# Kernel optimization log

Hardware: AMD Instinct MI355X
Metric: run time of the kernel (lower is better)

## Reference

```python
import jax, jax.numpy as jnp
import numpy as np
from jax import lax
jax.config.update('jax_enable_x64', True)

SR = 44100
BLOCK = 512
N_MELS = 80
N_ALLPASS = 256
N_HARM = 512
N_NOISE = 256
HID = 256
B = 16
NF = 400
T = NF * BLOCK
N_OUT = N_ALLPASS + N_HARM + N_NOISE


def upsample(sig, factor):
    # torch: interpolate(cat(sig, sig[-1:]), size=n*factor+1, mode='linear', align_corners=True)[:-1]
    b, n, c = sig.shape
    ext = jnp.concatenate([sig, sig[:, -1:]], axis=1)  # (b, n+1, c)
    w = (jnp.arange(factor, dtype=jnp.float32) / factor)[None, None, :, None]
    up = ext[:, :-1, None, :] * (1.0 - w) + ext[:, 1:, None, :] * w
    return up.reshape(b, n * factor, c)


def hann_periodic(n):
    return 0.5 - 0.5 * jnp.cos(2.0 * np.pi * jnp.arange(n, dtype=jnp.float32) / n)


def freq_impulse_response(mag, hann_window, half_width=None):
    # mag: (b, nf, m) complex -> ir: (b, nf, 2*(m-1)) in causal (rolled) form
    ir = jnp.fft.irfft(mag).astype(jnp.float32)
    n = ir.shape[-1]
    if hann_window:
        if half_width is None:
            w = jnp.roll(hann_periodic(n), n // 2)
            ir = jnp.roll(ir * w, n // 2, axis=-1)
        else:
            # dynamic hann window with per-frame half width (b, nf, 1)
            w = jnp.arange(-(n // 2), (n + 1) // 2, dtype=jnp.float32) / half_width
            w = jnp.where(w > 1.0, 0.0, w)
            w = (1.0 + jnp.cos(np.pi * w)) * 0.5
            ir = jnp.roll(ir, n // 2, axis=-1) * w
    else:
        ir = jnp.roll(ir, n // 2, axis=-1)
    return ir


def fft_convolve(audio, ir):
    b, t = audio.shape
    nf, ir_size = ir.shape[1], ir.shape[2]
    hop = t // nf
    frame = 2 * hop
    fft_size = frame + ir_size - 1
    chunks = jnp.pad(audio, ((0, 0), (hop, hop))).reshape(b, nf + 2, hop)
    frames = jnp.concatenate([chunks[:, :-1], chunks[:, 1:]], axis=-1)  # (b, nf+1, frame)
    bart = 1.0 - jnp.abs(2.0 * jnp.arange(frame, dtype=jnp.float32) / frame - 1.0)
    frames = frames * bart
    ir_ext = jnp.concatenate([ir, ir[:, -1:]], axis=1)  # repeat last IR frame
    out_f = jnp.fft.irfft(jnp.fft.rfft(frames, fft_size) * jnp.fft.rfft(ir_ext, fft_size), fft_size).astype(jnp.float32)
    n_out = nf + 1
    length = (n_out - 1) * hop + fft_size
    idx = (jnp.arange(n_out)[:, None] * hop + jnp.arange(fft_size)[None, :]).reshape(-1)
    out = jnp.zeros((b, length), jnp.float32).at[:, idx].add(out_f.reshape(b, -1))
    return out[:, hop:t + hop]


def conv1d_same(x, w, bias):
    y = lax.conv_general_dilated(x, w, (1,), [(1, 1)], dimension_numbers=('NCH', 'OIH', 'NCH'))
    return y + bias[None, :, None]


def mel2ctrl(mel, phase, conv1_w, conv1_b, gn_g, gn_b, conv2_w, conv2_b, phase_w, phase_b, ln_g, ln_b, out_w, out_b):
    h = conv1d_same(mel.transpose(0, 2, 1), conv1_w, conv1_b)  # (b, 256, nf)
    b, c, l = h.shape
    g = h.reshape(b, 4, c // 4, l)  # GroupNorm(4, 256)
    mu = g.mean((2, 3), keepdims=True)
    var = g.var((2, 3), keepdims=True)
    h = ((g - mu) / jnp.sqrt(var + 1e-5)).reshape(b, c, l)
    h = h * gn_g[None, :, None] + gn_b[None, :, None]
    h = jnp.where(h >= 0, h, 0.01 * h)  # LeakyReLU
    h = conv1d_same(h, conv2_w, conv2_b).transpose(0, 2, 1)  # (b, nf, 256)
    pe = jnp.concatenate([jnp.sin(phase), jnp.cos(phase)], axis=-1) @ phase_w.T + phase_b
    h = h + pe
    mu = h.mean(-1, keepdims=True)
    var = h.var(-1, keepdims=True)
    h = (h - mu) / jnp.sqrt(var + 1e-5) * ln_g + ln_b
    out = h @ out_w.T + out_b
    gd = out[..., :N_ALLPASS]
    hm = out[..., N_ALLPASS:N_ALLPASS + N_HARM]
    nm = out[..., N_ALLPASS + N_HARM:]
    return gd, hm, nm


def setup_inputs():
    key = jax.random.key(0)
    ks = jax.random.split(key, 8)
    s = 0.02
    return {
        'mel_frames': jax.random.normal(ks[0], (B, NF, N_MELS), jnp.float32),
        'f0_frames': jax.random.uniform(ks[1], (B, NF, 1), jnp.float32) * 400.0 + 100.0,
        'initial_phase': jnp.zeros((B, 1, 1), jnp.float32),
        'uniform_noise': jax.random.uniform(ks[2], (B, T), jnp.float32),
        'conv1_w': jax.random.normal(ks[3], (HID, N_MELS, 3), jnp.float32) * s,
        'conv1_b': jnp.zeros((HID,), jnp.float32),
        'gn_g': jnp.ones((HID,), jnp.float32),
        'gn_b': jnp.zeros((HID,), jnp.float32),
        'conv2_w': jax.random.normal(ks[4], (HID, HID, 3), jnp.float32) * s,
        'conv2_b': jnp.zeros((HID,), jnp.float32),
        'phase_w': jax.random.normal(ks[5], (HID, 2), jnp.float32) * s,
        'phase_b': jnp.zeros((HID,), jnp.float32),
        'ln_g': jnp.ones((HID,), jnp.float32),
        'ln_b': jnp.zeros((HID,), jnp.float32),
        'out_w': jax.random.normal(ks[6], (N_OUT, HID), jnp.float32) * s,
        'out_b': jnp.zeros((N_OUT,), jnp.float32),
    }


def reference(mel_frames, f0_frames, initial_phase, uniform_noise, conv1_w, conv1_b, gn_g, gn_b, conv2_w, conv2_b, phase_w, phase_b, ln_g, ln_b, out_w, out_b):
    f0 = upsample(f0_frames, BLOCK)  # (B, T, 1)
    # double-precision wrapped phase accumulation
    x = jnp.cumsum(f0.astype(jnp.float64) / SR, axis=1) + initial_phase.astype(jnp.float64) / (2.0 * np.pi)
    x = (x - jnp.round(x)).astype(jnp.float32)
    phase_frames = 2.0 * np.pi * x[:, ::BLOCK, :]  # (B, NF, 1)
    gd_raw, hm_raw, nm_raw = mel2ctrl(mel_frames, phase_frames, conv1_w, conv1_b, gn_g, gn_b, conv2_w, conv2_b, phase_w, phase_b, ln_g, ln_b, out_w, out_b)
    group_delay = np.pi * jnp.tanh(gd_raw)
    src_param = jnp.exp(hm_raw)
    noise_param = jnp.exp(nm_raw) / 128.0
    combtooth = jnp.sinc(SR * x / (f0 + 0.001))[..., 0]  # (B, T)
    allpass = jnp.exp(1j * jnp.cumsum(group_delay, axis=-1).astype(jnp.complex64))
    harmonic = fft_convolve(combtooth, freq_impulse_response(allpass, hann_window=False))
    half_width = 1.5 * SR / (f0_frames + 0.001)  # (B, NF, 1)
    harmonic = fft_convolve(harmonic, freq_impulse_response(src_param.astype(jnp.complex64), True, half_width))
    noise = uniform_noise * 2.0 - 1.0
    noise = fft_convolve(noise, freq_impulse_response(noise_param.astype(jnp.complex64), True, None))
    signal = harmonic + noise
    return signal, phase_frames, harmonic, noise
```

## Files before the change

### kernel.cpp

```cpp
#include <hip/hip_runtime.h>
#include <math.h>

#define BATCH 16
#define NF_ 400
#define TLEN 204800
#define NMELS 80
#define HID 256
#define SRD 44100.0

static constexpr size_t S_ = 1638400;
static constexpr size_t OFF_COMB = 0;
static constexpr size_t OFF_H1   = 2 * S_;
static constexpr size_t OFF_H2   = 3 * S_;
static constexpr size_t OFF_IR1  = 2 * S_;
static constexpr size_t OFF_PHI  = 4 * S_;
static constexpr size_t OFF_NSP  = 5 * S_;
static constexpr size_t OFF_HTMP = 4 * S_;
static constexpr size_t OFF_SRC  = 6 * S_;
static constexpr size_t OFF_IR3  = 6 * S_;
static constexpr size_t OFF_IR2  = 8 * S_;
static constexpr size_t OFF_FSUM = 12 * S_;
static constexpr size_t OFF_PREF = 12 * S_ + 12800;
static constexpr size_t OFF_GN   = 12 * S_ + 25600;

__device__ __forceinline__ float cs6_f0_at(const float* f0f, int b, int n, int k) {
    float a = f0f[b * NF_ + n];
    float c = f0f[b * NF_ + min(n + 1, NF_ - 1)];
    float w = (float)k * (1.0f / 512.0f);
    return __fadd_rn(__fmul_rn(a, 1.0f - w), __fmul_rn(c, w));
}

__global__ void cs6_fsum(const float* __restrict__ f0f, double* __restrict__ fsum) {
    int gid = blockIdx.x * blockDim.x + threadIdx.x;
    if (gid >= BATCH * NF_) return;
    int b = gid / NF_, n = gid % NF_;
    double s = 0.0;
    for (int k = 0; k < 512; ++k) s += (double)cs6_f0_at(f0f, b, n, k) / SRD;
    fsum[gid] = s;
}

__global__ void cs6_prefix(const double* __restrict__ fsum, double* __restrict__ pref) {
    int b = threadIdx.x;
    if (b >= BATCH) return;
    double run = 0.0;
    for (int n = 0; n < NF_; ++n) { pref[b * NF_ + n] = run; run += fsum[b * NF_ + n]; }
}

__global__ __launch_bounds__(512) void cs6_phase(const float* __restrict__ f0f,
        const float* __restrict__ ip, const double* __restrict__ pref,
        float* __restrict__ comb, float* __restrict__ phase_out) {
    __shared__ double sc[512];
    int b = blockIdx.x / NF_, n = blockIdx.x % NF_;
    int k = threadIdx.x;
    float f0 = cs6_f0_at(f0f, b, n, k);
    sc[k] = (double)f0 / SRD;
    __syncthreads();
    for (int off = 1; off < 512; off <<= 1) {
        double v = (k >= off) ? sc[k - off] : 0.0;
        __syncthreads();
        sc[k] += v;
        __syncthreads();
    }
    double xd = pref[b * NF_ + n] + sc[k] + (double)ip[b] / (2.0 * M_PI);
    xd -= rint(xd);
    float xf = (float)xd;
    double zd = 44100.0 * (double)xf / ((double)f0 + 0.001);
    double pz = M_PI * zd;
    comb[(size_t)b * TLEN + n * 512 + k] = (zd == 0.0) ? 1.0f : (float)(sin(pz) / pz);
    if (k == 0) phase_out[b * NF_ + n] = (float)(2.0 * M_PI * (double)xf);
}

__global__ __launch_bounds__(256) void cs6_conv1x3(const float* __restrict__ mel,
        const float* __restrict__ w1, const float* __restrict__ b1, float* __restrict__ h1) {
    __shared__ float m3[3][NMELS];
    int b = blockIdx.x / NF_, l = blockIdx.x % NF_;
    int tid = threadIdx.x;
    for (int i = tid; i < 3 * NMELS; i += 256) {
        int tap = i / NMELS, ic = i % NMELS;
        int li = l + tap - 1;
        m3[tap][ic] = (li >= 0 && li < NF_) ? mel[((size_t)b * NF_ + li) * NMELS + ic] : 0.0f;
    }
    __syncthreads();
    int oc = tid;
    double acc = (double)b1[oc];
    const float* wp = w1 + (size_t)oc * NMELS * 3;
    for (int ic = 0; ic < NMELS; ++ic)
        acc += (double)m3[0][ic] * (double)wp[ic * 3]
             + (double)m3[1][ic] * (double)wp[ic * 3 + 1]
             + (double)m3[2][ic] * (double)wp[ic * 3 + 2];
    h1[((size_t)b * NF_ + l) * HID + oc] = (float)acc;
}

__global__ __launch_bounds__(256) void cs6_gnstats(const float* __restrict__ h1, float* __restrict__ gn) {
    __shared__ double rs[256], rq[256];
    int b = blockIdx.x >> 2, g = blockIdx.x & 3;
    int tid = threadIdx.x;
    double s = 0.0, q = 0.0;
    for (int i = tid; i < 64 * NF_; i += 256) {
        int l = i >> 6, c = g * 64 + (i & 63);
        float v = h1[((size_t)b * NF_ + l) * HID + c];
        s += v; q += (double)v * v;
    }
    rs[tid] = s; rq[tid] = q;
    __syncthreads();
    for (int off = 128; off > 0; off >>= 1) {
        if (tid < off) { rs[tid] += rs[tid + off]; rq[tid] += rq[tid + off]; }
        __syncthreads();
    }
    if (tid == 0) {
        double mu = rs[0] / (64.0 * NF_);
        double var = rq[0] / (64.0 * NF_) - mu * mu;
        gn[blockIdx.x * 2] = (float)mu;
        gn[blockIdx.x * 2 + 1] = (float)(1.0 / sqrt(var + 1e-5));
    }
}

__global__ __launch_bounds__(256) void cs6_conv2ln(const float* __restrict__ h1,
        const float* __restrict__ gn, const float* __restrict__ gng, const float* __restrict__ gnb,
        const float* __restrict__ w2, const float* __restrict__ b2,
        const float* __restrict__ pw, const float* __restrict__ pb,
        const float* __restrict__ lng, const float* __restrict__ lnb,
        const float* __restrict__ phase, float* __restrict__ h2) {
    __shared__ float cols[10][HID];
    __shared__ double rsum[256], rsq[256];
    int b = blockIdx.x / 50, l0 = (blockIdx.x % 50) * 8;
    int tid = threadIdx.x;
    for (int i = tid; i < 10 * HID; i += 256) {
        int lc = i >> 8, c = i & 255;
        int l = l0 + lc - 1;
        float v = 0.0f;
        if (l >= 0 && l < NF_) {
            float hv = h1[((size_t)b * NF_ + l) * HID + c];
            int g = c >> 6;
            double vv = ((double)hv - (double)gn[(b * 4 + g) * 2]) * (double)gn[(b * 4 + g) * 2 + 1]
                        * (double)gng[c] + (double)gnb[c];
            v = (float)(vv >= 0.0 ? vv : 0.01 * vv);
        }
        cols[lc][c] = v;
    }
    __syncthreads();
    int oc = tid;
    double acc[8];
    #pragma unroll
    for (int lt = 0; lt < 8; ++lt) acc[lt] = (double)b2[oc];
    const float* wp = w2 + (size_t)oc * HID * 3;
    for (int ic = 0; ic < HID; ++ic) {
        double w0 = (double)wp[ic * 3], w1v = (double)wp[ic * 3 + 1], w2v = (double)wp[ic * 3 + 2];
        float cc[10];
        #pragma unroll
        for (int j = 0; j < 10; ++j) cc[j] = cols[j][ic];
        #pragma unroll
        for (int lt = 0; lt < 8; ++lt)
            acc[lt] += (double)cc[lt] * w0 + (double)cc[lt + 1] * w1v + (double)cc[lt + 2] * w2v;
    }
    for (int lt = 0; lt < 8; ++lt) {
        int l = l0 + lt;
        double ph = (double)phase[b * NF_ + l];
        double sp, cp; sincos(ph, &sp, &cp);
        double v = acc[lt] + sp * (double)pw[oc * 2] + cp * (double)pw[oc * 2 + 1] + (double)pb[oc];
        rsum[tid] = v; rsq[tid] = v * v;
        __syncthreads();
        for (int off = 128; off > 0; off >>= 1) {
            if (tid < off) { rsum[tid] += rsum[tid + off]; rsq[tid] += rsq[tid + off]; }
            __syncthreads();
        }
        double mu = rsum[0] * (1.0 / 256.0);
        double var = rsq[0] * (1.0 / 256.0) - mu * mu;
        double rstd = 1.0 / sqrt(var + 1e-5);
        __syncthreads();
        h2[((size_t)b * NF_ + l) * HID + oc] = (float)((v - mu) * rstd * (double)lng[oc] + (double)lnb[oc]);
    }
}

__global__ __launch_bounds__(256) void cs6_proj(const float* __restrict__ h2,
        const float* __restrict__ ow, const float* __restrict__ ob,
        float* __restrict__ phi, float* __restrict__ srcspec, float* __restrict__ nspec) {
    __shared__ float hrow[8][HID];
    __shared__ double ssc[256];
    int b = blockIdx.x / 50, l0 = (blockIdx.x % 50) * 8;
    int tid = threadIdx.x;
    for (int i = tid; i < 8 * HID; i += 256) {
        int lc = i >> 8, c = i & 255;
        hrow[lc][c] = h2[((size_t)b * NF_ + l0 + lc) * HID + c];
    }
    __syncthreads();
    double a0[8], a1[8], a2[8], a3[8];
    #pragma unroll
    for (int lt = 0; lt < 8; ++lt) {
        a0[lt] = (double)ob[tid];       a1[lt] = (double)ob[256 + tid];
        a2[lt] = (double)ob[512 + tid]; a3[lt] = (double)ob[768 + tid];
    }
    const float* w0p = ow + (size_t)tid * HID;
    const float* w1p = ow + (size_t)(256 + tid) * HID;
    const float* w2p = ow + (size_t)(512 + tid) * HID;
    const float* w3p = ow + (size_t)(768 + tid) * HID;
    for (int ic = 0; ic < HID; ++ic) {
        double w0 = (double)w0p[ic], w1v = (double)w1p[ic], w2v = (double)w2p[ic], w3v = (double)w3p[ic];
        #pragma unroll
        for (int lt = 0; lt < 8; ++lt) {
            double h = (double)hrow[lt][ic];
            a0[lt] += h * w0; a1[lt] += h * w1v; a2[lt] += h * w2v; a3[lt] += h * w3v;
        }
    }
    for (int lt = 0; lt < 8; ++lt) {
        size_t bl = (size_t)b * NF_ + (l0 + lt);
        double gdv = M_PI * tanh(a0[lt]);
        ssc[tid] = gdv;
        __syncthreads();
        for (int off = 1; off < 256; off <<= 1) {
            double v = (tid >= off) ? ssc[tid - off] : 0.0;
            __syncthreads();
            ssc[tid] += v;
            __syncthreads();
        }
        phi[bl * 256 + tid] = (float)ssc[tid];
        __syncthreads();
        srcspec[bl * 512 + tid] = (float)exp(a1[lt]);
        srcspec[bl * 512 + 256 + tid] = (float)exp(a2[lt]);
        nspec[bl * 256 + tid] = (float)(exp(a3[lt]) * (1.0 / 128.0));
    }
}

__global__ __launch_bounds__(256) void cs6_ir_allpass(const float* __restrict__ phi, float* __restrict__ ir1) {
    __shared__ double cph[256], sph[256];
    size_t bl = blockIdx.x;
    int tid = threadIdx.x;
    {
        double s, c; sincos((double)phi[bl * 256 + tid], &s, &c);
        cph[tid] = 2.0 * c; sph[tid] = 2.0 * s;
    }
    __syncthreads();
    for (int t = tid; t < 510; t += 256) {
        double ang = 2.0 * M_PI * (double)t / 510.0;
        double sr, cr; sincos(ang, &sr, &cr);
        double c = cr, s = sr;
        double acc = 0.5 * (cph[0] + ((t & 1) ? -cph[255] : cph[255]));
        for (int k = 1; k <= 254; ++k) {
            acc += cph[k] * c - sph[k] * s;
            double cn = c * cr - s * sr;
            double sn = s * cr + c * sr;
            c = cn; s = sn;
        }
        int j = t + 255; if (j >= 510) j -= 510;
        ir1[bl * 510 + j] = (float)(acc * (1.0 / 510.0));
    }
}

__device__ __forceinline__ double cs6_hw_win(int j, double hw) {
    double wv = (double)(j - 511) / hw;
    if (wv > 1.0) wv = 0.0;
    return (1.0 + cos(M_PI * wv)) * 0.5;
}

__global__ __launch_bounds__(256) void cs6_ir_src(const float* __restrict__ srcspec,
        const float* __restrict__ f0f, float* __restrict__ ir2) {
    __shared__ double sp[512];
    size_t bl = blockIdx.x;
    int b = blockIdx.x / NF_, l = blockIdx.x % NF_;
    int tid = threadIdx.x;
    sp[tid] = 2.0 * (double)srcspec[bl * 512 + tid];
    sp[tid + 256] = 2.0 * (double)srcspec[bl * 512 + 256 + tid];
    __syncthreads();
    double hw = 66150.0 / ((double)f0f[b * NF_ + l] + 0.001);
    for (int t = tid; t < 512; t += 256) {
        double ang = 2.0 * M_PI * (double)t / 1022.0;
        double sr, cr; sincos(ang, &sr, &cr);
        double c = cr, s = sr;
        double acc = 0.5 * (sp[0] + ((t & 1) ? -sp[511] : sp[511]));
        for (int k = 1; k <= 510; ++k) {
            acc += sp[k] * c;
            double cn = c * cr - s * sr;
            double sn = s * cr + c * sr;
            c = cn; s = sn;
        }
        double raw = acc * (1.0 / 1022.0);
        {
            int j = t + 511; if (j >= 1022) j -= 1022;
            ir2[bl * 1022 + j] = (float)(raw * cs6_hw_win(j, hw));
        }
        if (t >= 1 && t <= 510) {
            int j = 511 - t;
            ir2[bl * 1022 + j] = (float)(raw * cs6_hw_win(j, hw));
        }
    }
}

__global__ __launch_bounds__(256) void cs6_ir_noise(const float* __restrict__ nspec, float* __restrict__ ir3) {
    __shared__ double sp[256];
    size_t bl = blockIdx.x;
    int t = threadIdx.x;
    sp[t] = 2.0 * (double)nspec[bl * 256 + t];
    __syncthreads();
    double ang = 2.0 * M_PI * (double)t / 510.0;
    double sr, cr; sincos(ang, &sr, &cr);
    double c = cr, s = sr;
    double acc = 0.5 * (sp[0] + ((t & 1) ? -sp[255] : sp[255]));
    for (int k = 1; k <= 254; ++k) {
        acc += sp[k] * c;
        double cn = c * cr - s * sr;
        double sn = s * cr + c * sr;
        c = cn; s = sn;
    }
    double raw = acc * (1.0 / 510.0);
    {
        int j = t + 255; if (j >= 510) j -= 510;
        double win = 0.5 - 0.5 * cos(2.0 * M_PI * (double)j / 510.0);
        ir3[bl * 510 + j] = (float)(raw * win);
    }
    if (t >= 1 && t <= 254) {
        int j = 255 - t;
        double win = 0.5 - 0.5 * cos(2.0 * M_PI * (double)j / 510.0);
        ir3[bl * 510 + j] = (float)(raw * win);
    }
}

template<int IRS, int NFRM, int MOFF>
__global__ __launch_bounds__(256) void cs6_conv(const float* __restrict__ audio,
        const float* __restrict__ ir, float* __restrict__ out, float scale, float shift) {
    __shared__ float fr[NFRM][1024];
    __shared__ float irp[NFRM][IRS + 8];
    int b = blockIdx.x / 200, q = blockIdx.x % 200;
    int t0 = q * 1024;
    int m_lo = 2 * q + MOFF;
    int tid = threadIdx.x;
    for (int i = tid; i < NFRM * 1024; i += 256) {
        int fi = i >> 10, k = i & 1023;
        int m = m_lo + fi;
        int idx = (m << 9) + k - 512;
        float v = 0.0f;
        if (m >= 0 && m <= 400 && idx >= 0 && idx < TLEN)
            v = audio[(size_t)b * TLEN + idx] * scale + shift;
        float bart = 1.0f - fabsf((float)k * (1.0f / 512.0f) - 1.0f);
        fr[fi][k] = v * bart;
    }
    for (int i = tid; i < NFRM * (IRS + 8); i += 256) {
        int fi = i / (IRS + 8), j = i % (IRS + 8);
        int jj = j - 4;
        int m = m_lo + fi;
        float v = 0.0f;
        if (jj >= 0 && jj < IRS && m >= 0 && m <= 400)
            v = ir[((size_t)b * NF_ + min(m, 399)) * IRS + jj];
        irp[fi][j] = v;
    }
    __syncthreads();
    int tb = t0 + tid * 4;
    int s0 = tb + 512;
    float acc0 = 0, acc1 = 0, acc2 = 0, acc3 = 0;
    #pragma unroll
    for (int fi = 0; fi < NFRM; ++fi) {
        int m = m_lo + fi;
        if (m < 0 || m > 400) continue;
        int d0 = s0 - (m << 9);
        int k_lo = max(0, d0 - (IRS - 1));
        int k_hi = min(1023, d0 + 3);
        if (k_lo > k_hi) continue;
        const float* irow = &irp[fi][4];
        int jb = d0 - k_lo;
        float w1v = irow[jb + 1], w2v = irow[jb + 2], w3v = irow[jb + 3];
        for (int k = k_lo; k <= k_hi; ++k) {
            float w0v = irow[d0 - k];
            float f = fr[fi][k];
            acc0 += f * w0v; acc1 += f * w1v; acc2 += f * w2v; acc3 += f * w3v;
            w3v = w2v; w2v = w1v; w1v = w0v;
        }
    }
    *(float4*)(out + (size_t)b * TLEN + tb) = make_float4(acc0, acc1, acc2, acc3);
}

__global__ void cs6_add(const float* __restrict__ a, const float* __restrict__ b,
                        float* __restrict__ o, int n4) {
    int i = blockIdx.x * blockDim.x + threadIdx.x;
    if (i < n4) {
        float4 x = ((const float4*)a)[i];
        float4 y = ((const float4*)b)[i];
        ((float4*)o)[i] = make_float4(x.x + y.x, x.y + y.y, x.z + y.z, x.w + y.w);
    }
}

extern "C" void kernel_launch(void* const* d_in, const int* in_sizes, int n_in,
                              void* d_out, int out_size, void* d_ws, size_t ws_size,
                              hipStream_t stream) {
    const float* mel   = (const float*)d_in[0];
    const float* f0f   = (const float*)d_in[1];
    const float* ip    = (const float*)d_in[2];
    const float* unoi  = (const float*)d_in[3];
    const float* w1    = (const float*)d_in[4];
    const float* b1    = (const float*)d_in[5];
    const float* gng   = (const float*)d_in[6];
    const float* gnb   = (const float*)d_in[7];
    const float* w2    = (const float*)d_in[8];
    const float* b2    = (const float*)d_in[9];
    const float* pw    = (const float*)d_in[10];
    const float* pb    = (const float*)d_in[11];
    const float* lng   = (const float*)d_in[12];
    const float* lnb   = (const float*)d_in[13];
    const float* ow    = (const float*)d_in[14];
    const float* ob    = (const float*)d_in[15];
    float* out = (float*)d_out;
    float* ws  = (float*)d_ws;

    float*  comb = ws + OFF_COMB;
    float*  h1   = ws + OFF_H1;
    float*  h2   = ws + OFF_H2;
    float*  ir1  = ws + OFF_IR1;
    float*  phi  = ws + OFF_PHI;
    float*  nsp  = ws + OFF_NSP;
    float*  htmp = ws + OFF_HTMP;
    float*  ssp  = ws + OFF_SRC;
    float*  ir3  = ws + OFF_IR3;
    float*  ir2  = ws + OFF_IR2;
    double* fsum = (double*)(ws + OFF_FSUM);
    double* pref = (double*)(ws + OFF_PREF);
    float*  gn   = ws + OFF_GN;

    float* out_sig   = out;
    float* out_phase = out + (size_t)BATCH * TLEN;
    float* out_harm  = out_phase + BATCH * NF_;
    float* out_noise = out_harm + (size_t)BATCH * TLEN;

    cs6_fsum<<<25, 256, 0, stream>>>(f0f, fsum);
    cs6_prefix<<<1, 16, 0, stream>>>(fsum, pref);
    cs6_phase<<<BATCH * NF_, 512, 0, stream>>>(f0f, ip, pref, comb, out_phase);
    cs6_conv1x3<<<BATCH * NF_, 256, 0, stream>>>(mel, w1, b1, h1);
    cs6_gnstats<<<64, 256, 0, stream>>>(h1, gn);
    cs6_conv2ln<<<BATCH * 50, 256, 0, stream>>>(h1, gn, gng, gnb, w2, b2, pw, pb, lng, lnb, out_phase, h2);
    cs6_proj<<<BATCH * 50, 256, 0, stream>>>(h2, ow, ob, phi, ssp, nsp);
    cs6_ir_allpass<<<BATCH * NF_, 256, 0, stream>>>(phi, ir1);
    cs6_ir_src<<<BATCH * NF_, 256, 0, stream>>>(ssp, f0f, ir2);
    cs6_ir_noise<<<BATCH * NF_, 256, 0, stream>>>(nsp, ir3);
    cs6_conv<510, 4, -1><<<BATCH * 200, 256, 0, stream>>>(comb, ir1, htmp, 1.0f, 0.0f);
    cs6_conv<1022, 5, -2><<<BATCH * 200, 256, 0, stream>>>(htmp, ir2, out_harm, 1.0f, 0.0f);
    cs6_conv<510, 4, -1><<<BATCH * 200, 256, 0, stream>>>(unoi, ir3, out_noise, 2.0f, -1.0f);
    cs6_add<<<(BATCH * TLEN / 4 + 255) / 256, 256, 0, stream>>>(out_harm, out_noise, out_sig, BATCH * TLEN / 4);
}
```

Before: 2.806 ms.

## Use float IR synthesis with re-anchored rotations and vectorized wave-uniform conv loops

The IR synthesis kernels switch from double to float for the DFT accumulation and windows. The twiddle recurrence runs in float but is re-anchored from a double recurrence every 16 steps to limit drift. The direct convolution kernel now stores the IR reversed and padded in shared memory and runs a wave-uniform loop over float4 chunks with a register-rotated sliding window. This removes per-thread divergent loop bounds and scalar LDS loads. Each wave now covers the union range of its lanes, so lanes do extra multiply-adds against zero padding, and float accumulation adds some rounding error.

Result: no change. 2.853 ms (+1.7%).

```diff
diff --git a/kernel.cpp b/kernel.cpp
--- a/kernel.cpp
+++ b/kernel.cpp
@@ -23,36 +23,36 @@
 static constexpr size_t OFF_PREF = 12 * S_ + 12800;
 static constexpr size_t OFF_GN   = 12 * S_ + 25600;
 
-__device__ __forceinline__ float cs6_f0_at(const float* f0f, int b, int n, int k) {
+__device__ __forceinline__ float cs7_f0_at(const float* f0f, int b, int n, int k) {
     float a = f0f[b * NF_ + n];
     float c = f0f[b * NF_ + min(n + 1, NF_ - 1)];
     float w = (float)k * (1.0f / 512.0f);
     return __fadd_rn(__fmul_rn(a, 1.0f - w), __fmul_rn(c, w));
 }
 
-__global__ void cs6_fsum(const float* __restrict__ f0f, double* __restrict__ fsum) {
+__global__ void cs7_fsum(const float* __restrict__ f0f, double* __restrict__ fsum) {
     int gid = blockIdx.x * blockDim.x + threadIdx.x;
     if (gid >= BATCH * NF_) return;
     int b = gid / NF_, n = gid % NF_;
     double s = 0.0;
-    for (int k = 0; k < 512; ++k) s += (double)cs6_f0_at(f0f, b, n, k) / SRD;
+    for (int k = 0; k < 512; ++k) s += (double)cs7_f0_at(f0f, b, n, k) / SRD;
     fsum[gid] = s;
 }
 
-__global__ void cs6_prefix(const double* __restrict__ fsum, double* __restrict__ pref) {
+__global__ void cs7_prefix(const double* __restrict__ fsum, double* __restrict__ pref) {
     int b = threadIdx.x;
     if (b >= BATCH) return;
     double run = 0.0;
     for (int n = 0; n < NF_; ++n) { pref[b * NF_ + n] = run; run += fsum[b * NF_ + n]; }
 }
 
-__global__ __launch_bounds__(512) void cs6_phase(const float* __restrict__ f0f,
+__global__ __launch_bounds__(512) void cs7_phase(const float* __restrict__ f0f,
         const float* __restrict__ ip, const double* __restrict__ pref,
         float* __restrict__ comb, float* __restrict__ phase_out) {
     __shared__ double sc[512];
     int b = blockIdx.x / NF_, n = blockIdx.x % NF_;
     int k = threadIdx.x;
-    float f0 = cs6_f0_at(f0f, b, n, k);
+    float f0 = cs7_f0_at(f0f, b, n, k);
     sc[k] = (double)f0 / SRD;
     __syncthreads();
     for (int off = 1; off < 512; off <<= 1) {
@@ -70,7 +70,7 @@
     if (k == 0) phase_out[b * NF_ + n] = (float)(2.0 * M_PI * (double)xf);
 }
 
-__global__ __launch_bounds__(256) void cs6_conv1x3(const float* __restrict__ mel,
+__global__ __launch_bounds__(256) void cs7_conv1x3(const float* __restrict__ mel,
         const float* __restrict__ w1, const float* __restrict__ b1, float* __restrict__ h1) {
     __shared__ float m3[3][NMELS];
     int b = blockIdx.x / NF_, l = blockIdx.x % NF_;
@@ -91,7 +91,7 @@
     h1[((size_t)b * NF_ + l) * HID + oc] = (float)acc;
 }
 
-__global__ __launch_bounds__(256) void cs6_gnstats(const float* __restrict__ h1, float* __restrict__ gn) {
+__global__ __launch_bounds__(256) void cs7_gnstats(const float* __restrict__ h1, float* __restrict__ gn) {
     __shared__ double rs[256], rq[256];
     int b = blockIdx.x >> 2, g = blockIdx.x & 3;
     int tid = threadIdx.x;
@@ -115,7 +115,7 @@
     }
 }
 
-__global__ __launch_bounds__(256) void cs6_conv2ln(const float* __restrict__ h1,
+__global__ __launch_bounds__(256) void cs7_conv2ln(const float* __restrict__ h1,
         const float* __restrict__ gn, const float* __restrict__ gng, const float* __restrict__ gnb,
         const float* __restrict__ w2, const float* __restrict__ b2,
         const float* __restrict__ pw, const float* __restrict__ pb,
@@ -172,7 +172,7 @@
     }
 }
 
-__global__ __launch_bounds__(256) void cs6_proj(const float* __restrict__ h2,
+__global__ __launch_bounds__(256) void cs7_proj(const float* __restrict__ h2,
         const float* __restrict__ ow, const float* __restrict__ ob,
         float* __restrict__ phi, float* __restrict__ srcspec, float* __restrict__ nspec) {
     __shared__ float hrow[8][HID];
@@ -221,153 +221,198 @@
     }
 }
 
-__global__ __launch_bounds__(256) void cs6_ir_allpass(const float* __restrict__ phi, float* __restrict__ ir1) {
-    __shared__ double cph[256], sph[256];
+__global__ __launch_bounds__(256) void cs7_ir_allpass(const float* __restrict__ phi, float* __restrict__ ir1) {
+    __shared__ float cph[256], sph[256];
     size_t bl = blockIdx.x;
     int tid = threadIdx.x;
     {
-        double s, c; sincos((double)phi[bl * 256 + tid], &s, &c);
-        cph[tid] = 2.0 * c; sph[tid] = 2.0 * s;
+        float ph = phi[bl * 256 + tid];
+        cph[tid] = 2.0f * cosf(ph); sph[tid] = 2.0f * sinf(ph);
     }
     __syncthreads();
     for (int t = tid; t < 510; t += 256) {
         double ang = 2.0 * M_PI * (double)t / 510.0;
-        double sr, cr; sincos(ang, &sr, &cr);
-        double c = cr, s = sr;
-        double acc = 0.5 * (cph[0] + ((t & 1) ? -cph[255] : cph[255]));
-        for (int k = 1; k <= 254; ++k) {
-            acc += cph[k] * c - sph[k] * s;
-            double cn = c * cr - s * sr;
-            double sn = s * cr + c * sr;
-            c = cn; s = sn;
+        double srd_, crd; sincos(ang, &srd_, &crd);
+        double sj, cj;    sincos(16.0 * ang, &sj, &cj);
+        float crf = (float)crd, srf = (float)srd_;
+        double cD = crd, sD = srd_;
+        float acc = 0.5f * (cph[0] + ((t & 1) ? -cph[255] : cph[255]));
+        for (int k0 = 1; k0 <= 254; k0 += 16) {
+            float c = (float)cD, s = (float)sD;
+            int ke = min(k0 + 16, 255);
+            for (int k = k0; k < ke; ++k) {
+                acc += cph[k] * c - sph[k] * s;
+                float cn = c * crf - s * srf;
+                float sn = s * crf + c * srf;
+                c = cn; s = sn;
+            }
+            double nc = cD * cj - sD * sj;
+            double ns = sD * cj + cD * sj;
+            cD = nc; sD = ns;
         }
         int j = t + 255; if (j >= 510) j -= 510;
-        ir1[bl * 510 + j] = (float)(acc * (1.0 / 510.0));
-    }
-}
-
-__device__ __forceinline__ double cs6_hw_win(int j, double hw) {
-    double wv = (double)(j - 511) / hw;
-    if (wv > 1.0) wv = 0.0;
-    return (1.0 + cos(M_PI * wv)) * 0.5;
-}
-
-__global__ __launch_bounds__(256) void cs6_ir_src(const float* __restrict__ srcspec,
+        ir1[bl * 510 + j] = acc * (1.0f / 510.0f);
+    }
+}
+
+__device__ __forceinline__ float cs7_hw_win(int j, float hw) {
+    float wv = (float)(j - 511) / hw;
+    if (wv > 1.0f) wv = 0.0f;
+    return (1.0f + cosf((float)M_PI * wv)) * 0.5f;
+}
+
+__global__ __launch_bounds__(256) void cs7_ir_src(const float* __restrict__ srcspec,
         const float* __restrict__ f0f, float* __restrict__ ir2) {
-    __shared__ double sp[512];
+    __shared__ float sp[512];
     size_t bl = blockIdx.x;
     int b = blockIdx.x / NF_, l = blockIdx.x % NF_;
     int tid = threadIdx.x;
-    sp[tid] = 2.0 * (double)srcspec[bl * 512 + tid];
-    sp[tid + 256] = 2.0 * (double)srcspec[bl * 512 + 256 + tid];
-    __syncthreads();
-    double hw = 66150.0 / ((double)f0f[b * NF_ + l] + 0.001);
+    sp[tid] = 2.0f * srcspec[bl * 512 + tid];
+    sp[tid + 256] = 2.0f * srcspec[bl * 512 + 256 + tid];
+    __syncthreads();
+    float hw = 66150.0f / (f0f[b * NF_ + l] + 0.001f);
     for (int t = tid; t < 512; t += 256) {
         double ang = 2.0 * M_PI * (double)t / 1022.0;
-        double sr, cr; sincos(ang, &sr, &cr);
-        double c = cr, s = sr;
-        double acc = 0.5 * (sp[0] + ((t & 1) ? -sp[511] : sp[511]));
-        for (int k = 1; k <= 510; ++k) {
-            acc += sp[k] * c;
-            double cn = c * cr - s * sr;
-            double sn = s * cr + c * sr;
-            c = cn; s = sn;
-        }
-        double raw = acc * (1.0 / 1022.0);
+        double srd_, crd; sincos(ang, &srd_, &crd);
+        double sj, cj;    sincos(16.0 * ang, &sj, &cj);
+        float crf = (float)crd, srf = (float)srd_;
+        double cD = crd, sD = srd_;
+        float acc = 0.5f * (sp[0] + ((t & 1) ? -sp[511] : sp[511]));
+        for (int k0 = 1; k0 <= 510; k0 += 16) {
+            float c = (float)cD, s = (float)sD;
+            int ke = min(k0 + 16, 511);
+            for (int k = k0; k < ke; ++k) {
+                acc += sp[k] * c;
+                float cn = c * crf - s * srf;
+                float sn = s * crf + c * srf;
+                c = cn; s = sn;
+            }
+            double nc = cD * cj - sD * sj;
+            double ns = sD * cj + cD * sj;
+            cD = nc; sD = ns;
+        }
+        float raw = acc * (1.0f / 1022.0f);
         {
             int j = t + 511; if (j >= 1022) j -= 1022;
-            ir2[bl * 1022 + j] = (float)(raw * cs6_hw_win(j, hw));
+            ir2[bl * 1022 + j] = raw * cs7_hw_win(j, hw);
         }
         if (t >= 1 && t <= 510) {
             int j = 511 - t;
-            ir2[bl * 1022 + j] = (float)(raw * cs6_hw_win(j, hw));
-        }
-    }
-}
-
-__global__ __launch_bounds__(256) void cs6_ir_noise(const float* __restrict__ nspec, float* __restrict__ ir3) {
-    __shared__ double sp[256];
+            ir2[bl * 1022 + j] = raw * cs7_hw_win(j, hw);
+        }
+    }
+}
+
+__global__ __launch_bounds__(256) void cs7_ir_noise(const float* __restrict__ nspec, float* __restrict__ ir3) {
+    __shared__ float sp[256];
     size_t bl = blockIdx.x;
     int t = threadIdx.x;
-    sp[t] = 2.0 * (double)nspec[bl * 256 + t];
+    sp[t] = 2.0f * nspec[bl * 256 + t];
     __syncthreads();
     double ang = 2.0 * M_PI * (double)t / 510.0;
-    double sr, cr; sincos(ang, &sr, &cr);
-    double c = cr, s = sr;
-    double acc = 0.5 * (sp[0] + ((t & 1) ? -sp[255] : sp[255]));
-    for (int k = 1; k <= 254; ++k) {
-        acc += sp[k] * c;
-        double cn = c * cr - s * sr;
-        double sn = s * cr + c * sr;
-        c = cn; s = sn;
-    }
-    double raw = acc * (1.0 / 510.0);
+    double srd_, crd; sincos(ang, &srd_, &crd);
+    double sj, cj;    sincos(16.0 * ang, &sj, &cj);
+    float crf = (float)crd, srf = (float)srd_;
+    double cD = crd, sD = srd_;
+    float acc = 0.5f * (sp[0] + ((t & 1) ? -sp[255] : sp[255]));
+    for (int k0 = 1; k0 <= 254; k0 += 16) {
+        float c = (float)cD, s = (float)sD;
+        int ke = min(k0 + 16, 255);
+        for (int k = k0; k < ke; ++k) {
+            acc += sp[k] * c;
+            float cn = c * crf - s * srf;
+            float sn = s * crf + c * srf;
+            c = cn; s = sn;
+        }
+        double nc = cD * cj - sD * sj;
+        double ns = sD * cj + cD * sj;
+        cD = nc; sD = ns;
+    }
+    float raw = acc * (1.0f / 510.0f);
     {
         int j = t + 255; if (j >= 510) j -= 510;
-        double win = 0.5 - 0.5 * cos(2.0 * M_PI * (double)j / 510.0);
-        ir3[bl * 510 + j] = (float)(raw * win);
+        float win = 0.5f - 0.5f * cosf((float)(2.0 * M_PI) * (float)j / 510.0f);
+        ir3[bl * 510 + j] = raw * win;
     }
     if (t >= 1 && t <= 254) {
         int j = 255 - t;
-        double win = 0.5 - 0.5 * cos(2.0 * M_PI * (double)j / 510.0);
-        ir3[bl * 510 + j] = (float)(raw * win);
+        float win = 0.5f - 0.5f * cosf((float)(2.0 * M_PI) * (float)j / 510.0f);
+        ir3[bl * 510 + j] = raw * win;
     }
 }
 
 template<int IRS, int NFRM, int MOFF>
-__global__ __launch_bounds__(256) void cs6_conv(const float* __restrict__ audio,
+__global__ __launch_bounds__(256) void cs7_conv(const float* __restrict__ audio,
         const float* __restrict__ ir, float* __restrict__ out, float scale, float shift) {
-    __shared__ float fr[NFRM][1024];
-    __shared__ float irp[NFRM][IRS + 8];
+    constexpr int PAD = 264;
+    constexpr int W   = (IRS + 2 * PAD + 3) & ~3;
+    constexpr int FRW = 1040;
+    __shared__ float4 sir4[NFRM][W / 4];
+    __shared__ float4 fr4[NFRM][FRW / 4];
+    float* sir = (float*)sir4;
+    float* frp = (float*)fr4;
     int b = blockIdx.x / 200, q = blockIdx.x % 200;
     int t0 = q * 1024;
     int m_lo = 2 * q + MOFF;
     int tid = threadIdx.x;
-    for (int i = tid; i < NFRM * 1024; i += 256) {
-        int fi = i >> 10, k = i & 1023;
-        int m = m_lo + fi;
-        int idx = (m << 9) + k - 512;
-        float v = 0.0f;
-        if (m >= 0 && m <= 400 && idx >= 0 && idx < TLEN)
-            v = audio[(size_t)b * TLEN + idx] * scale + shift;
-        float bart = 1.0f - fabsf((float)k * (1.0f / 512.0f) - 1.0f);
-        fr[fi][k] = v * bart;
-    }
-    for (int i = tid; i < NFRM * (IRS + 8); i += 256) {
-        int fi = i / (IRS + 8), j = i % (IRS + 8);
-        int jj = j - 4;
+
+    for (int i = tid; i < NFRM * FRW; i += 256) {
+        int fi = i / FRW, kk = i - fi * FRW;
+        int k = kk - 6;
+        float sv = 0.0f;
+        if (k >= 0 && k < 1024) {
+            int m = m_lo + fi;
+            int idx = (m << 9) + k - 512;
+            float v = 0.0f;
+            if (m >= 0 && m <= 400 && idx >= 0 && idx < TLEN)
+                v = audio[(size_t)b * TLEN + idx] * scale + shift;
+            float bart = 1.0f - fabsf((float)k * (1.0f / 512.0f) - 1.0f);
+            sv = v * bart;
+        }
+        frp[fi * FRW + kk] = sv;
+    }
+    for (int i = tid; i < NFRM * W; i += 256) {
+        int fi = i / W, x = i - fi * W;
+        int j = (IRS - 1 + PAD) - x;
         int m = m_lo + fi;
         float v = 0.0f;
-        if (jj >= 0 && jj < IRS && m >= 0 && m <= 400)
-            v = ir[((size_t)b * NF_ + min(m, 399)) * IRS + jj];
-        irp[fi][j] = v;
-    }
-    __syncthreads();
+        if (j >= 0 && j < IRS && m >= 0 && m <= 400)
+            v = ir[((size_t)b * NF_ + min(m, 399)) * IRS + j];
+        sir[fi * W + x] = v;
+    }
+    __syncthreads();
+
     int tb = t0 + tid * 4;
-    int s0 = tb + 512;
+    int wtid0 = tid & ~63;
     float acc0 = 0, acc1 = 0, acc2 = 0, acc3 = 0;
     #pragma unroll
     for (int fi = 0; fi < NFRM; ++fi) {
         int m = m_lo + fi;
         if (m < 0 || m > 400) continue;
-        int d0 = s0 - (m << 9);
-        int k_lo = max(0, d0 - (IRS - 1));
-        int k_hi = min(1023, d0 + 3);
-        if (k_lo > k_hi) continue;
-        const float* irow = &irp[fi][4];
-        int jb = d0 - k_lo;
-        float w1v = irow[jb + 1], w2v = irow[jb + 2], w3v = irow[jb + 3];
-        for (int k = k_lo; k <= k_hi; ++k) {
-            float w0v = irow[d0 - k];
-            float f = fr[fi][k];
-            acc0 += f * w0v; acc1 += f * w1v; acc2 += f * w2v; acc3 += f * w3v;
-            w3v = w2v; w2v = w1v; w1v = w0v;
+        int d0w = t0 + wtid0 * 4 + 512 - (m << 9);
+        int klo = max(0, d0w - (IRS - 1));
+        int khi = min(1023, d0w + 255);
+        if (klo > khi) continue;
+        int kc0 = (((klo - 2) & ~3) + 2);
+        int nch = ((khi - kc0) >> 2) + 1;
+        int d0  = t0 + tid * 4 + 512 - (m << 9);
+        const float4* sp = (const float4*)(sir + fi * W + ((IRS + PAD - 4) - d0 + kc0));
+        const float4* fp = (const float4*)(frp + fi * FRW + 6 + kc0);
+        float4 A = sp[0];
+        for (int c = 0; c < nch; ++c) {
+            float4 B = sp[c + 1];
+            float4 F = fp[c];
+            acc3 += F.x * A.x; acc2 += F.x * A.y; acc1 += F.x * A.z; acc0 += F.x * A.w;
+            acc3 += F.y * A.y; acc2 += F.y * A.z; acc1 += F.y * A.w; acc0 += F.y * B.x;
+            acc3 += F.z * A.z; acc2 += F.z * A.w; acc1 += F.z * B.x; acc0 += F.z * B.y;
+            acc3 += F.w * A.w; acc2 += F.w * B.x; acc1 += F.w * B.y; acc0 += F.w * B.z;
+            A = B;
         }
     }
     *(float4*)(out + (size_t)b * TLEN + tb) = make_float4(acc0, acc1, acc2, acc3);
 }
 
-__global__ void cs6_add(const float* __restrict__ a, const float* __restrict__ b,
+__global__ void cs7_add(const float* __restrict__ a, const float* __restrict__ b,
                         float* __restrict__ o, int n4) {
     int i = blockIdx.x * blockDim.x + threadIdx.x;
     if (i < n4) {
@@ -418,18 +463,18 @@
     float* out_harm  = out_phase + BATCH * NF_;
     float* out_noise = out_harm + (size_t)BATCH * TLEN;
 
-    cs6_fsum<<<25, 256, 0, stream>>>(f0f, fsum);
-    cs6_prefix<<<1, 16, 0, stream>>>(fsum, pref);
-    cs6_phase<<<BATCH * NF_, 512, 0, stream>>>(f0f, ip, pref, comb, out_phase);
-    cs6_conv1x3<<<BATCH * NF_, 256, 0, stream>>>(mel, w1, b1, h1);
-    cs6_gnstats<<<64, 256, 0, stream>>>(h1, gn);
-    cs6_conv2ln<<<BATCH * 50, 256, 0, stream>>>(h1, gn, gng, gnb, w2, b2, pw, pb, lng, lnb, out_phase, h2);
-    cs6_proj<<<BATCH * 50, 256, 0, stream>>>(h2, ow, ob, phi, ssp, nsp);
-    cs6_ir_allpass<<<BATCH * NF_, 256, 0, stream>>>(phi, ir1);
-    cs6_ir_src<<<BATCH * NF_, 256, 0, stream>>>(ssp, f0f, ir2);
-    cs6_ir_noise<<<BATCH * NF_, 256, 0, stream>>>(nsp, ir3);
-    cs6_conv<510, 4, -1><<<BATCH * 200, 256, 0, stream>>>(comb, ir1, htmp, 1.0f, 0.0f);
-    cs6_conv<1022, 5, -2><<<BATCH * 200, 256, 0, stream>>>(htmp, ir2, out_harm, 1.0f, 0.0f);
-    cs6_conv<510, 4, -1><<<BATCH * 200, 256, 0, stream>>>(unoi, ir3, out_noise, 2.0f, -1.0f);
-    cs6_add<<<(BATCH * TLEN / 4 + 255) / 256, 256, 0, stream>>>(out_harm, out_noise, out_sig, BATCH * TLEN / 4);
-}
+    cs7_fsum<<<25, 256, 0, stream>>>(f0f, fsum);
+    cs7_prefix<<<1, 16, 0, stream>>>(fsum, pref);
+    cs7_phase<<<BATCH * NF_, 512, 0, stream>>>(f0f, ip, pref, comb, out_phase);
+    cs7_conv1x3<<<BATCH * NF_, 256, 0, stream>>>(mel, w1, b1, h1);
+    cs7_gnstats<<<64, 256, 0, stream>>>(h1, gn);
+    cs7_conv2ln<<<BATCH * 50, 256, 0, stream>>>(h1, gn, gng, gnb, w2, b2, pw, pb, lng, lnb, out_phase, h2);
+    cs7_proj<<<BATCH * 50, 256, 0, stream>>>(h2, ow, ob, phi, ssp, nsp);
+    cs7_ir_allpass<<<BATCH * NF_, 256, 0, stream>>>(phi, ir1);
+    cs7_ir_src<<<BATCH * NF_, 256, 0, stream>>>(ssp, f0f, ir2);
+    cs7_ir_noise<<<BATCH * NF_, 256, 0, stream>>>(nsp, ir3);
+    cs7_conv<510, 4, -1><<<BATCH * 200, 256, 0, stream>>>(comb, ir1, htmp, 1.0f, 0.0f);
+    cs7_conv<1022, 5, -2><<<BATCH * 200, 256, 0, stream>>>(htmp, ir2, out_harm, 1.0f, 0.0f);
+    cs7_conv<510, 4, -1><<<BATCH * 200, 256, 0, stream>>>(unoi, ir3, out_noise, 2.0f, -1.0f);
+    cs7_add<<<(BATCH * TLEN / 4 + 255) / 256, 256, 0, stream>>>(out_harm, out_noise, out_sig, BATCH * TLEN / 4);
+}
```
